# Kernel tuning notes

Hardware: AMD Instinct MI355X
Metric: run time of the kernel (lower is better)

The kernel has to match this reference:

```python
import jax, jax.numpy as jnp
import numpy as np

C = 256
C8 = C // 8  # query/key channels
B, T, W, H = 4, 8, 32, 32


def setup_inputs() -> dict:
    key = jax.random.key(0)
    ks = jax.random.split(key, 8)
    s = 0.05
    return {
        "x": jax.random.normal(ks[0], (B, C, T, W, H), dtype=jnp.float32),
        "wq": jax.random.normal(ks[1], (C8, C), dtype=jnp.float32) * s,
        "bq": jax.random.normal(ks[2], (C8,), dtype=jnp.float32) * s,
        "wk": jax.random.normal(ks[3], (C8, C), dtype=jnp.float32) * s,
        "bk": jax.random.normal(ks[4], (C8,), dtype=jnp.float32) * s,
        "wv": jax.random.normal(ks[5], (C, C), dtype=jnp.float32) * s,
        "bv": jax.random.normal(ks[6], (C,), dtype=jnp.float32) * s,
        "gamma": jax.random.normal(ks[7], (1,), dtype=jnp.float32),
    }


def reference(x, wq, bq, wk, bk, wv, bv, gamma):
    b, c, t, w, h = x.shape
    n = w * h
    # Faithful to torch: x.view(-1, c, w, h) is a row-major reinterpretation
    xr = jnp.reshape(x, (-1, c, n))  # (m, C, N), m = B*T
    # 1x1 convs == per-pixel linear projections
    q = jnp.einsum("oc,mcn->mno", wq, xr) + bq            # (m, N, C8)
    k = jnp.einsum("oc,mcn->mon", wk, xr) + bk[:, None]   # (m, C8, N)
    v = jnp.einsum("oc,mcn->mon", wv, xr) + bv[:, None]   # (m, C, N)
    energy = jnp.einsum("mic,mcj->mij", q, k)             # (m, N, N), unscaled
    attention = jax.nn.softmax(energy, axis=-1)
    out = jnp.einsum("mcn,mnj->mcj", v, attention)        # V @ A (as in torch code)
    out = jnp.reshape(out, (b, c, t, w, h))
    return gamma * out + x
```

## Files before the change

kernel.cpp:

```cpp
#include <hip/hip_runtime.h>

#define MB    32
#define CCH   256
#define QCH   32
#define NPIX  1024
#define SLICE (CCH * NPIX)
#define L2E   1.44269504088896340736f
#define SHIFT 32.0f

typedef __bf16          bf16x8 __attribute__((ext_vector_type(8)));
typedef __bf16          bf16x4 __attribute__((ext_vector_type(4)));
typedef float           f32x4  __attribute__((ext_vector_type(4)));
typedef unsigned int    u32x4  __attribute__((ext_vector_type(4)));
typedef unsigned short  u16x4  __attribute__((ext_vector_type(4)));

__device__ __forceinline__ unsigned short f2bf(float f) {
    unsigned int u = __builtin_bit_cast(unsigned int, f);
    u += 0x7FFFu + ((u >> 16) & 1u);
    return (unsigned short)(u >> 16);
}
__device__ __forceinline__ u16x4 cvt4(float a, float b, float c, float d) {
    bf16x4 v = { (__bf16)a, (__bf16)b, (__bf16)c, (__bf16)d };
    return __builtin_bit_cast(u16x4, v);
}
__device__ __forceinline__ float bf2f(unsigned short u) {
    unsigned int v = (unsigned int)u << 16;
    return __builtin_bit_cast(float, v);
}
__device__ __forceinline__ bf16x8 ldfrag(const unsigned short* p) {
    u32x4 u = *(const u32x4*)p;
    return __builtin_bit_cast(bf16x8, u);
}

#define WB_OFF  0u
#define QT_OFF  262144u
#define KT_OFF  2359296u
#define V_OFF   4456448u
#define A2F_OFF 21233664u
#define PU_OFF  21364736u
#define WS_NEED 88473600u

__global__ __launch_bounds__(256) void k_prep_w(
    const float* __restrict__ wq, const float* __restrict__ wk,
    const float* __restrict__ wv, unsigned short* __restrict__ Wb)
{
    int i4 = (blockIdx.x * 256 + threadIdx.x) * 4;
    int o = i4 >> 8, c = i4 & 255;
    const float* src = (o < 32) ? wq + (size_t)o * CCH + c
                     : (o < 64) ? wk + (size_t)(o - 32) * CCH + c
                                : wv + (size_t)(o - 64) * CCH + c;
    float4 v = *(const float4*)src;
    *(u16x4*)(Wb + i4) = cvt4(v.x, v.y, v.z, v.w);
}

__global__ __launch_bounds__(256) void k_proj(
    const float* __restrict__ x, const unsigned short* __restrict__ Wb,
    const float* __restrict__ bq, const float* __restrict__ bk,
    const float* __restrict__ bv,
    unsigned short* __restrict__ Qt, unsigned short* __restrict__ Kt,
    unsigned short* __restrict__ V)
{
    __shared__ unsigned short Xs[64 * 268];

    const int t = threadIdx.x, lane = t & 63, w = t >> 6;
    const int lj = lane & 15, q = lane >> 4;
    const int n0 = blockIdx.x * 64;
    const int mi = blockIdx.y;
    const float* xp = x + (size_t)mi * SLICE;

#pragma unroll
    for (int r = 0; r < 8; ++r) {
        int job = t + r * 256;
        int cp = job >> 4;
        int seg = job & 15;
        float4 va = *(const float4*)(xp + (size_t)(2 * cp) * NPIX + n0 + seg * 4);
        float4 vb = *(const float4*)(xp + (size_t)(2 * cp + 1) * NPIX + n0 + seg * 4);
        u16x4 da = cvt4(va.x, va.y, va.z, va.w);
        u16x4 db = cvt4(vb.x, vb.y, vb.z, vb.w);
#pragma unroll
        for (int e = 0; e < 4; ++e) {
            unsigned pk = (unsigned)da[e] | ((unsigned)db[e] << 16);
            *(unsigned*)&Xs[(seg * 4 + e) * 268 + 2 * cp] = pk;
        }
    }
    __syncthreads();

    f32x4 acc[5][4];
#pragma unroll
    for (int i = 0; i < 5; ++i)
#pragma unroll
        for (int b = 0; b < 4; ++b) acc[i][b] = (f32x4){0.f, 0.f, 0.f, 0.f};

    const unsigned short* wbase = Wb + (size_t)(w * 16 + lj) * CCH + q * 8;
    const unsigned short* xbase = &Xs[lj * 268 + q * 8];

#pragma unroll 2
    for (int kc = 0; kc < CCH; kc += 32) {
        bf16x8 a[5];
#pragma unroll
        for (int i = 0; i < 5; ++i)
            a[i] = ldfrag(wbase + (size_t)i * 64 * CCH + kc);
        bf16x8 xb[4];
#pragma unroll
        for (int b = 0; b < 4; ++b)
            xb[b] = ldfrag(xbase + b * 16 * 268 + kc);
#pragma unroll
        for (int i = 0; i < 5; ++i)
#pragma unroll
            for (int b = 0; b < 4; ++b)
                acc[i][b] = (i == 0)
                    ? __builtin_amdgcn_mfma_f32_16x16x32_bf16(a[i], xb[b], acc[i][b], 0, 0, 0)
                    : __builtin_amdgcn_mfma_f32_16x16x32_bf16(xb[b], a[i], acc[i][b], 0, 0, 0);
    }

#pragma unroll
    for (int i = 0; i < 5; ++i) {
        if (i == 0) {
            const int ob = w * 16 + 4 * q;
            if (w < 2) {
                unsigned short* Qp = Qt + (size_t)mi * NPIX * QCH;
                float b0 = bq[ob], b1 = bq[ob + 1], b2 = bq[ob + 2], b3 = bq[ob + 3];
#pragma unroll
                for (int b = 0; b < 4; ++b) {
                    int n = n0 + b * 16 + lj;
                    *(u16x4*)(Qp + (size_t)n * QCH + ob) =
                        cvt4((acc[i][b][0] + b0) * L2E, (acc[i][b][1] + b1) * L2E,
                             (acc[i][b][2] + b2) * L2E, (acc[i][b][3] + b3) * L2E);
                }
            } else {
                unsigned short* Kp = Kt + (size_t)mi * NPIX * QCH;
                int o2 = ob - 32;
                float b0 = bk[o2], b1 = bk[o2 + 1], b2 = bk[o2 + 2], b3 = bk[o2 + 3];
#pragma unroll
                for (int b = 0; b < 4; ++b) {
                    int n = n0 + b * 16 + lj;
                    *(u16x4*)(Kp + (size_t)n * QCH + o2) =
                        cvt4(acc[i][b][0] + b0, acc[i][b][1] + b1,
                             acc[i][b][2] + b2, acc[i][b][3] + b3);
                }
            }
        } else {
            unsigned short* Vw = V + (size_t)mi * SLICE;
            const int c16 = w + 4 * (i - 1);
            const float bb = bv[c16 * 16 + lj];
            const int n05 = n0 >> 5;
#pragma unroll
            for (int b = 0; b < 4; ++b) {
                const int l = lj | (((b & 1) * 2 + (q >> 1)) << 4);
                size_t base = ((size_t)(c16 * 32 + n05 + (b >> 1)) * 64 + l) * 8 + (q & 1) * 4;
                *(u16x4*)(Vw + base) = cvt4(acc[i][b][0] + bb, acc[i][b][1] + bb,
                                            acc[i][b][2] + bb, acc[i][b][3] + bb);
            }
        }
    }
}

__global__ __launch_bounds__(256) void k_stats(
    const unsigned short* __restrict__ Qt, const unsigned short* __restrict__ Kt,
    float* __restrict__ a2f)
{
    const int t = threadIdx.x, lane = t & 63, w = t >> 6;
    const int lj = lane & 15, q = lane >> 4;
    const int n16 = blockIdx.x * 64 + w * 16;
    const int mi = blockIdx.y;
    const unsigned short* Qp = Qt + (size_t)mi * NPIX * QCH;
    const unsigned short* Kp = Kt + (size_t)mi * NPIX * QCH;

    bf16x8 qa = ldfrag(Qp + (size_t)(n16 + lj) * QCH + q * 8);

    float s[4] = { 0.f, 0.f, 0.f, 0.f };
#pragma unroll 8
    for (int jc = 0; jc < NPIX; jc += 16) {
        bf16x8 kb = ldfrag(Kp + (size_t)(jc + lj) * QCH + q * 8);
        f32x4 z = (f32x4){0.f, 0.f, 0.f, 0.f};
        f32x4 e = __builtin_amdgcn_mfma_f32_16x16x32_bf16(qa, kb, z, 0, 0, 0);
#pragma unroll
        for (int r = 0; r < 4; ++r) s[r] += exp2f(e[r] - SHIFT);
    }
#pragma unroll
    for (int msk = 1; msk <= 8; msk <<= 1)
#pragma unroll
        for (int r = 0; r < 4; ++r) s[r] += __shfl_xor(s[r], msk, 64);
    if (lj == 0) {
        float* apo = a2f + (size_t)mi * NPIX;
#pragma unroll
        for (int r = 0; r < 4; ++r)
            apo[n16 + 4 * q + r] = SHIFT + log2f(s[r]);
    }
}

__global__ __launch_bounds__(256) void k_pu(
    const unsigned short* __restrict__ Qt, const unsigned short* __restrict__ Kt,
    const float* __restrict__ a2f, unsigned short* __restrict__ Pu)
{
    __shared__ unsigned short Ps[4][32][36];

    const int t = threadIdx.x, lane = t & 63, w = t >> 6;
    const int lj = lane & 15, q = lane >> 4;
    const int nb = blockIdx.x >> 2;
    const int jh = blockIdx.x & 3;
    const int nw = nb * 128 + w * 32;
    const int mi = blockIdx.y;
    const unsigned short* Qp = Qt + (size_t)mi * NPIX * QCH;
    const unsigned short* Kp = Kt + (size_t)mi * NPIX * QCH;
    const float* ap = a2f + (size_t)mi * NPIX;
    unsigned short* Pup = Pu + (size_t)mi * NPIX * NPIX;

    bf16x8 qa[2];
    f32x4  a4[2];
#pragma unroll
    for (int h = 0; h < 2; ++h) {
        qa[h] = ldfrag(Qp + (size_t)(nw + h * 16 + lj) * QCH + q * 8);
        a4[h] = *(const f32x4*)(ap + nw + h * 16 + 4 * q);
    }

    const int jbeg = jh * 256;
#pragma unroll 2
    for (int jc = jbeg; jc < jbeg + 256; jc += 32) {
#pragma unroll
        for (int f = 0; f < 2; ++f) {
            bf16x8 kb = ldfrag(Kp + (size_t)(jc + f * 16 + lj) * QCH + q * 8);
#pragma unroll
            for (int h = 0; h < 2; ++h) {
                f32x4 z = (f32x4){0.f, 0.f, 0.f, 0.f};
                f32x4 e = __builtin_amdgcn_mfma_f32_16x16x32_bf16(qa[h], kb, z, 0, 0, 0);
                *(u16x4*)&Ps[w][f * 16 + lj][h * 16 + 4 * q] =
                    cvt4(exp2f(e[0] - a4[h][0]), exp2f(e[1] - a4[h][1]),
                         exp2f(e[2] - a4[h][2]), exp2f(e[3] - a4[h][3]));
            }
        }
#pragma unroll
        for (int f = 0; f < 2; ++f) {
            u32x4 bfrag = *(const u32x4*)&Ps[w][f * 16 + lj][q * 8];
            *(u32x4*)(Pup + ((size_t)((jc >> 4) + f) * 32 + (nw >> 5)) * 512 + lane * 8) = bfrag;
        }
    }
}

__global__ __launch_bounds__(256, 4) void k_gemm_out(
    const float* __restrict__ x, const float* __restrict__ gamma,
    const unsigned short* __restrict__ Vf, const unsigned short* __restrict__ Pu,
    float* __restrict__ out)
{
    __shared__ unsigned short Vs[2][4096];

    const int b = blockIdx.x;
    const int mi  = (b & 7) | ((b >> 8) << 3);
    const int sub = (b >> 3) & 31;
    const int j0  = (sub & 7) * 128;
    const int cb  = sub >> 3;

    const int t = threadIdx.x, lane = t & 63, w = t >> 6;
    const int lj = lane & 15, q = lane >> 4;
    const int jw = j0 + w * 32;

    const unsigned short* Vp  = Vf + (size_t)mi * SLICE;
    const unsigned short* Pup = Pu + (size_t)mi * NPIX * NPIX
                              + ((size_t)(jw >> 4) * 32) * 512 + lane * 8;

    const int fs = t >> 5;
    const int ln0 = (t & 31) * 2;
    const unsigned short* vsrc0 = Vp
        + ((size_t)((cb * 4 + (fs & 3)) * 32) + (fs >> 2)) * 512 + ln0 * 8;

    f32x4 acc[4][2];
#pragma unroll
    for (int ci = 0; ci < 4; ++ci)
#pragma unroll
        for (int f = 0; f < 2; ++f) acc[ci][f] = (f32x4){0.f, 0.f, 0.f, 0.f};

    {
        u32x4 d0 = *(const u32x4*)vsrc0;
        u32x4 d1 = *(const u32x4*)(vsrc0 + 8);
        *(u32x4*)&Vs[0][fs * 512 + ln0 * 8] = d0;
        *(u32x4*)&Vs[0][fs * 512 + ln0 * 8 + 8] = d1;
    }
    bf16x8 pf[2][2], pfN[2][2];
#pragma unroll
    for (int h = 0; h < 2; ++h)
#pragma unroll
        for (int f = 0; f < 2; ++f) {
            pf[h][f]  = ldfrag(Pup + f * 16384 + (size_t)h * 512);
            pfN[h][f] = ldfrag(Pup + f * 16384 + (size_t)(2 + h) * 512);
        }
    __syncthreads();

    int p = 0;
    for (int nc = 0; nc < NPIX; nc += 64, p ^= 1) {
        const int n1 = (nc + 64) & (NPIX - 1);
        const int n2 = (nc + 128) & (NPIX - 1);
        const unsigned short* vs = vsrc0 + (size_t)(n1 >> 6) * 1024;
        u32x4 nv0 = *(const u32x4*)vs;
        u32x4 nv1 = *(const u32x4*)(vs + 8);
        bf16x8 pf2[2][2];
#pragma unroll
        for (int h = 0; h < 2; ++h)
#pragma unroll
            for (int f = 0; f < 2; ++f)
                pf2[h][f] = ldfrag(Pup + f * 16384 + ((size_t)(n2 >> 5) + h) * 512);

        __builtin_amdgcn_s_setprio(1);
#pragma unroll
        for (int h = 0; h < 2; ++h) {
#pragma unroll
            for (int ci = 0; ci < 4; ++ci) {
                bf16x8 vfr = ldfrag(&Vs[p][(h * 4 + ci) * 512 + lane * 8]);
#pragma unroll
                for (int f = 0; f < 2; ++f)
                    acc[ci][f] = __builtin_amdgcn_mfma_f32_16x16x32_bf16(vfr, pf[h][f], acc[ci][f], 0, 0, 0);
            }
        }
        __builtin_amdgcn_s_setprio(0);

        *(u32x4*)&Vs[p ^ 1][fs * 512 + ln0 * 8] = nv0;
        *(u32x4*)&Vs[p ^ 1][fs * 512 + ln0 * 8 + 8] = nv1;
        __syncthreads();
#pragma unroll
        for (int h = 0; h < 2; ++h)
#pragma unroll
            for (int f = 0; f < 2; ++f) { pf[h][f] = pfN[h][f]; pfN[h][f] = pf2[h][f]; }
    }

    const float g = gamma[0];
    const size_t obase = (size_t)mi * SLICE;
#pragma unroll
    for (int ci = 0; ci < 4; ++ci) {
#pragma unroll
        for (int f = 0; f < 2; ++f) {
#pragma unroll
            for (int r = 0; r < 4; ++r) {
                int c = cb * 64 + ci * 16 + 4 * q + r;
                int j = jw + f * 16 + lj;
                size_t off = obase + (size_t)c * NPIX + j;
                out[off] = g * acc[ci][f][r] + x[off];
            }
        }
    }
}

__global__ __launch_bounds__(256) void k_attn_out(
    const float* __restrict__ x, const float* __restrict__ gamma,
    const unsigned short* __restrict__ Qt, const unsigned short* __restrict__ Kt,
    const unsigned short* __restrict__ Vf, const float* __restrict__ a2f,
    float* __restrict__ out)
{
    __shared__ unsigned short Vs[2][8 * 512];
    __shared__ unsigned short Ps[4][32][36];

    const int b = blockIdx.x;
    const int mi  = (b & 7) | ((b >> 7) << 3);
    const int sub = (b >> 3) & 15;
    const int j0  = (sub & 7) * 128;
    const int cb  = sub >> 3;

    const int t = threadIdx.x, lane = t & 63, w = t >> 6;
    const int lj = lane & 15, q = lane >> 4;
    const int jw = j0 + w * 32;

    const unsigned short* Qp = Qt + (size_t)mi * NPIX * QCH;
    const unsigned short* Kp = Kt + (size_t)mi * NPIX * QCH;
    const unsigned short* Vp = Vf + (size_t)mi * SLICE;
    const float* ap = a2f + (size_t)mi * NPIX;

    bf16x8 kb[2];
#pragma unroll
    for (int sj = 0; sj < 2; ++sj)
        kb[sj] = ldfrag(Kp + (size_t)(jw + sj * 16 + lj) * QCH + q * 8);

    const int ctl = t >> 5, ln0 = (t & 31) * 2;
    const unsigned short* vsrc0 = Vp + ((size_t)(cb * 8 + ctl) * 32) * 512 + ln0 * 8;

    f32x4 acc[8][2];
#pragma unroll
    for (int ci = 0; ci < 8; ++ci)
#pragma unroll
        for (int ji = 0; ji < 2; ++ji) acc[ci][ji] = (f32x4){0.f, 0.f, 0.f, 0.f};

    {
        u32x4 d0 = *(const u32x4*)vsrc0;
        u32x4 d1 = *(const u32x4*)(vsrc0 + 8);
        *(u32x4*)&Vs[0][ctl * 512 + ln0 * 8] = d0;
        *(u32x4*)&Vs[0][ctl * 512 + ln0 * 8 + 8] = d1;
    }
    bf16x8 qa_n[2];
    f32x4  a4_n[2];
#pragma unroll
    for (int sn = 0; sn < 2; ++sn) {
        qa_n[sn] = ldfrag(Qp + (size_t)(sn * 16 + lj) * QCH + q * 8);
        a4_n[sn] = *(const f32x4*)(ap + sn * 16 + 4 * q);
    }
    __syncthreads();

    int p = 0;
    for (int nc = 0; nc < NPIX; nc += 32, p ^= 1) {
        const int nn = (nc + 32) & (NPIX - 1);
        const unsigned short* vsrc = vsrc0 + (size_t)(nn >> 5) * 512;
        u32x4 nv0 = *(const u32x4*)vsrc;
        u32x4 nv1 = *(const u32x4*)(vsrc + 8);

        bf16x8 qa0 = qa_n[0], qa1 = qa_n[1];
        f32x4 a40 = a4_n[0], a41 = a4_n[1];
#pragma unroll
        for (int sj = 0; sj < 2; ++sj) {
            f32x4 z = (f32x4){0.f, 0.f, 0.f, 0.f};
            f32x4 e0 = __builtin_amdgcn_mfma_f32_16x16x32_bf16(qa0, kb[sj], z, 0, 0, 0);
            f32x4 e1 = __builtin_amdgcn_mfma_f32_16x16x32_bf16(qa1, kb[sj], z, 0, 0, 0);
            *(u16x4*)&Ps[w][sj * 16 + lj][4 * q] =
                cvt4(exp2f(e0[0] - a40[0]), exp2f(e0[1] - a40[1]),
                     exp2f(e0[2] - a40[2]), exp2f(e0[3] - a40[3]));
            *(u16x4*)&Ps[w][sj * 16 + lj][16 + 4 * q] =
                cvt4(exp2f(e1[0] - a41[0]), exp2f(e1[1] - a41[1]),
                     exp2f(e1[2] - a41[2]), exp2f(e1[3] - a41[3]));
        }
#pragma unroll
        for (int sn = 0; sn < 2; ++sn) {
            qa_n[sn] = ldfrag(Qp + (size_t)(nn + sn * 16 + lj) * QCH + q * 8);
            a4_n[sn] = *(const f32x4*)(ap + nn + sn * 16 + 4 * q);
        }

        bf16x8 pf[2];
#pragma unroll
        for (int ji = 0; ji < 2; ++ji)
            pf[ji] = ldfrag(&Ps[w][ji * 16 + lj][q * 8]);
#pragma unroll
        for (int ci = 0; ci < 8; ++ci) {
            bf16x8 vfr = ldfrag(&Vs[p][ci * 512 + lane * 8]);
#pragma unroll
            for (int ji = 0; ji < 2; ++ji)
                acc[ci][ji] = __builtin_amdgcn_mfma_f32_16x16x32_bf16(vfr, pf[ji], acc[ci][ji], 0, 0, 0);
        }

        *(u32x4*)&Vs[p ^ 1][ctl * 512 + ln0 * 8] = nv0;
        *(u32x4*)&Vs[p ^ 1][ctl * 512 + ln0 * 8 + 8] = nv1;
        __syncthreads();
    }

    const float g = gamma[0];
    const size_t obase = (size_t)mi * SLICE;
#pragma unroll
    for (int ci = 0; ci < 8; ++ci) {
#pragma unroll
        for (int ji = 0; ji < 2; ++ji) {
#pragma unroll
            for (int r = 0; r < 4; ++r) {
                int c = cb * 128 + ci * 16 + 4 * q + r;
                int j = jw + ji * 16 + lj;
                size_t off = obase + (size_t)c * NPIX + j;
                out[off] = g * acc[ci][ji][r] + x[off];
            }
        }
    }
}

extern "C" void kernel_launch(void* const* d_in, const int* in_sizes, int n_in,
                              void* d_out, int out_size, void* d_ws, size_t ws_size,
                              hipStream_t stream)
{
    const float* x     = (const float*)d_in[0];
    const float* wq    = (const float*)d_in[1];
    const float* bq    = (const float*)d_in[2];
    const float* wk    = (const float*)d_in[3];
    const float* bk    = (const float*)d_in[4];
    const float* wv    = (const float*)d_in[5];
    const float* bv    = (const float*)d_in[6];
    const float* gamma = (const float*)d_in[7];
    float* out = (float*)d_out;

    char* wsb = (char*)d_ws;
    unsigned short* Wb = (unsigned short*)(wsb + WB_OFF);
    unsigned short* Qt = (unsigned short*)(wsb + QT_OFF);
    unsigned short* Kt = (unsigned short*)(wsb + KT_OFF);
    unsigned short* V  = (unsigned short*)(wsb + V_OFF);
    float*          a2 = (float*)(wsb + A2F_OFF);
    unsigned short* Pu = (unsigned short*)(wsb + PU_OFF);

    k_prep_w<<<80, 256, 0, stream>>>(wq, wk, wv, Wb);
    k_proj<<<dim3(NPIX / 64, MB), 256, 0, stream>>>(x, Wb, bq, bk, bv, Qt, Kt, V);
    k_stats<<<dim3(NPIX / 64, MB), 256, 0, stream>>>(Qt, Kt, a2);

    if (ws_size >= (size_t)WS_NEED) {
        k_pu<<<dim3(32, MB), 256, 0, stream>>>(Qt, Kt, a2, Pu);
        k_gemm_out<<<1024, 256, 0, stream>>>(x, gamma, V, Pu, out);
    } else {
        k_attn_out<<<512, 256, 0, stream>>>(x, gamma, Qt, Kt, V, a2, out);
    }
}
```

Measured before the change: 163.1 us.

## Drop materialized P path; use fused attention kernel with 64-pixel double-buffered V tiles

Removes the two-kernel path that writes the full normalized attention matrix to workspace in bf16 and reads it back in a separate GEMM. Every call now runs the fused kernel, which recomputes the attention probabilities on the fly from Q, K and the precomputed log-sum statistics. That kernel now processes 64 pixels per pipeline step instead of 32, with a larger double-buffered V tile, prefetched Q fragments and priority hints around the MFMA loop. The aim is to avoid the large global write and reread of P, at the cost of fewer blocks (512 vs 1024) and more exp work per block.

```diff
diff --git a/kernel.cpp b/kernel.cpp
--- a/kernel.cpp
+++ b/kernel.cpp
@@ -37,8 +37,6 @@
 #define KT_OFF  2359296u
 #define V_OFF   4456448u
 #define A2F_OFF 21233664u
-#define PU_OFF  21364736u
-#define WS_NEED 88473600u
 
 __global__ __launch_bounds__(256) void k_prep_w(
     const float* __restrict__ wq, const float* __restrict__ wk,
@@ -189,162 +187,13 @@
     }
 }
 
-__global__ __launch_bounds__(256) void k_pu(
-    const unsigned short* __restrict__ Qt, const unsigned short* __restrict__ Kt,
-    const float* __restrict__ a2f, unsigned short* __restrict__ Pu)
-{
-    __shared__ unsigned short Ps[4][32][36];
-
-    const int t = threadIdx.x, lane = t & 63, w = t >> 6;
-    const int lj = lane & 15, q = lane >> 4;
-    const int nb = blockIdx.x >> 2;
-    const int jh = blockIdx.x & 3;
-    const int nw = nb * 128 + w * 32;
-    const int mi = blockIdx.y;
-    const unsigned short* Qp = Qt + (size_t)mi * NPIX * QCH;
-    const unsigned short* Kp = Kt + (size_t)mi * NPIX * QCH;
-    const float* ap = a2f + (size_t)mi * NPIX;
-    unsigned short* Pup = Pu + (size_t)mi * NPIX * NPIX;
-
-    bf16x8 qa[2];
-    f32x4  a4[2];
-#pragma unroll
-    for (int h = 0; h < 2; ++h) {
-        qa[h] = ldfrag(Qp + (size_t)(nw + h * 16 + lj) * QCH + q * 8);
-        a4[h] = *(const f32x4*)(ap + nw + h * 16 + 4 * q);
-    }
-
-    const int jbeg = jh * 256;
-#pragma unroll 2
-    for (int jc = jbeg; jc < jbeg + 256; jc += 32) {
-#pragma unroll
-        for (int f = 0; f < 2; ++f) {
-            bf16x8 kb = ldfrag(Kp + (size_t)(jc + f * 16 + lj) * QCH + q * 8);
-#pragma unroll
-            for (int h = 0; h < 2; ++h) {
-                f32x4 z = (f32x4){0.f, 0.f, 0.f, 0.f};
-                f32x4 e = __builtin_amdgcn_mfma_f32_16x16x32_bf16(qa[h], kb, z, 0, 0, 0);
-                *(u16x4*)&Ps[w][f * 16 + lj][h * 16 + 4 * q] =
-                    cvt4(exp2f(e[0] - a4[h][0]), exp2f(e[1] - a4[h][1]),
-                         exp2f(e[2] - a4[h][2]), exp2f(e[3] - a4[h][3]));
-            }
-        }
-#pragma unroll
-        for (int f = 0; f < 2; ++f) {
-            u32x4 bfrag = *(const u32x4*)&Ps[w][f * 16 + lj][q * 8];
-            *(u32x4*)(Pup + ((size_t)((jc >> 4) + f) * 32 + (nw >> 5)) * 512 + lane * 8) = bfrag;
-        }
-    }
-}
-
-__global__ __launch_bounds__(256, 4) void k_gemm_out(
-    const float* __restrict__ x, const float* __restrict__ gamma,
-    const unsigned short* __restrict__ Vf, const unsigned short* __restrict__ Pu,
-    float* __restrict__ out)
-{
-    __shared__ unsigned short Vs[2][4096];
-
-    const int b = blockIdx.x;
-    const int mi  = (b & 7) | ((b >> 8) << 3);
-    const int sub = (b >> 3) & 31;
-    const int j0  = (sub & 7) * 128;
-    const int cb  = sub >> 3;
-
-    const int t = threadIdx.x, lane = t & 63, w = t >> 6;
-    const int lj = lane & 15, q = lane >> 4;
-    const int jw = j0 + w * 32;
-
-    const unsigned short* Vp  = Vf + (size_t)mi * SLICE;
-    const unsigned short* Pup = Pu + (size_t)mi * NPIX * NPIX
-                              + ((size_t)(jw >> 4) * 32) * 512 + lane * 8;
-
-    const int fs = t >> 5;
-    const int ln0 = (t & 31) * 2;
-    const unsigned short* vsrc0 = Vp
-        + ((size_t)((cb * 4 + (fs & 3)) * 32) + (fs >> 2)) * 512 + ln0 * 8;
-
-    f32x4 acc[4][2];
-#pragma unroll
-    for (int ci = 0; ci < 4; ++ci)
-#pragma unroll
-        for (int f = 0; f < 2; ++f) acc[ci][f] = (f32x4){0.f, 0.f, 0.f, 0.f};
-
-    {
-        u32x4 d0 = *(const u32x4*)vsrc0;
-        u32x4 d1 = *(const u32x4*)(vsrc0 + 8);
-        *(u32x4*)&Vs[0][fs * 512 + ln0 * 8] = d0;
-        *(u32x4*)&Vs[0][fs * 512 + ln0 * 8 + 8] = d1;
-    }
-    bf16x8 pf[2][2], pfN[2][2];
-#pragma unroll
-    for (int h = 0; h < 2; ++h)
-#pragma unroll
-        for (int f = 0; f < 2; ++f) {
-            pf[h][f]  = ldfrag(Pup + f * 16384 + (size_t)h * 512);
-            pfN[h][f] = ldfrag(Pup + f * 16384 + (size_t)(2 + h) * 512);
-        }
-    __syncthreads();
-
-    int p = 0;
-    for (int nc = 0; nc < NPIX; nc += 64, p ^= 1) {
-        const int n1 = (nc + 64) & (NPIX - 1);
-        const int n2 = (nc + 128) & (NPIX - 1);
-        const unsigned short* vs = vsrc0 + (size_t)(n1 >> 6) * 1024;
-        u32x4 nv0 = *(const u32x4*)vs;
-        u32x4 nv1 = *(const u32x4*)(vs + 8);
-        bf16x8 pf2[2][2];
-#pragma unroll
-        for (int h = 0; h < 2; ++h)
-#pragma unroll
-            for (int f = 0; f < 2; ++f)
-                pf2[h][f] = ldfrag(Pup + f * 16384 + ((size_t)(n2 >> 5) + h) * 512);
-
-        __builtin_amdgcn_s_setprio(1);
-#pragma unroll
-        for (int h = 0; h < 2; ++h) {
-#pragma unroll
-            for (int ci = 0; ci < 4; ++ci) {
-                bf16x8 vfr = ldfrag(&Vs[p][(h * 4 + ci) * 512 + lane * 8]);
-#pragma unroll
-                for (int f = 0; f < 2; ++f)
-                    acc[ci][f] = __builtin_amdgcn_mfma_f32_16x16x32_bf16(vfr, pf[h][f], acc[ci][f], 0, 0, 0);
-            }
-        }
-        __builtin_amdgcn_s_setprio(0);
-
-        *(u32x4*)&Vs[p ^ 1][fs * 512 + ln0 * 8] = nv0;
-        *(u32x4*)&Vs[p ^ 1][fs * 512 + ln0 * 8 + 8] = nv1;
-        __syncthreads();
-#pragma unroll
-        for (int h = 0; h < 2; ++h)
-#pragma unroll
-            for (int f = 0; f < 2; ++f) { pf[h][f] = pfN[h][f]; pfN[h][f] = pf2[h][f]; }
-    }
-
-    const float g = gamma[0];
-    const size_t obase = (size_t)mi * SLICE;
-#pragma unroll
-    for (int ci = 0; ci < 4; ++ci) {
-#pragma unroll
-        for (int f = 0; f < 2; ++f) {
-#pragma unroll
-            for (int r = 0; r < 4; ++r) {
-                int c = cb * 64 + ci * 16 + 4 * q + r;
-                int j = jw + f * 16 + lj;
-                size_t off = obase + (size_t)c * NPIX + j;
-                out[off] = g * acc[ci][f][r] + x[off];
-            }
-        }
-    }
-}
-
-__global__ __launch_bounds__(256) void k_attn_out(
+__global__ __launch_bounds__(256) void k_fused(
     const float* __restrict__ x, const float* __restrict__ gamma,
     const unsigned short* __restrict__ Qt, const unsigned short* __restrict__ Kt,
     const unsigned short* __restrict__ Vf, const float* __restrict__ a2f,
     float* __restrict__ out)
 {
-    __shared__ unsigned short Vs[2][8 * 512];
+    __shared__ unsigned short Vs[2][8192];
     __shared__ unsigned short Ps[4][32][36];
 
     const int b = blockIdx.x;
@@ -367,8 +216,8 @@
     for (int sj = 0; sj < 2; ++sj)
         kb[sj] = ldfrag(Kp + (size_t)(jw + sj * 16 + lj) * QCH + q * 8);
 
-    const int ctl = t >> 5, ln0 = (t & 31) * 2;
-    const unsigned short* vsrc0 = Vp + ((size_t)(cb * 8 + ctl) * 32) * 512 + ln0 * 8;
+    const int fs = t >> 5, ln0 = (t & 31) * 2;
+    const unsigned short* vsrc0 = Vp + ((size_t)(cb * 8 + fs) * 32) * 512 + ln0 * 8;
 
     f32x4 acc[8][2];
 #pragma unroll
@@ -377,62 +226,82 @@
         for (int ji = 0; ji < 2; ++ji) acc[ci][ji] = (f32x4){0.f, 0.f, 0.f, 0.f};
 
     {
-        u32x4 d0 = *(const u32x4*)vsrc0;
-        u32x4 d1 = *(const u32x4*)(vsrc0 + 8);
-        *(u32x4*)&Vs[0][ctl * 512 + ln0 * 8] = d0;
-        *(u32x4*)&Vs[0][ctl * 512 + ln0 * 8 + 8] = d1;
-    }
-    bf16x8 qa_n[2];
-    f32x4  a4_n[2];
-#pragma unroll
-    for (int sn = 0; sn < 2; ++sn) {
-        qa_n[sn] = ldfrag(Qp + (size_t)(sn * 16 + lj) * QCH + q * 8);
-        a4_n[sn] = *(const f32x4*)(ap + sn * 16 + 4 * q);
-    }
+        u32x4 a0 = *(const u32x4*)(vsrc0);
+        u32x4 a1 = *(const u32x4*)(vsrc0 + 8);
+        u32x4 b0 = *(const u32x4*)(vsrc0 + 512);
+        u32x4 b1 = *(const u32x4*)(vsrc0 + 520);
+        *(u32x4*)&Vs[0][fs * 512 + ln0 * 8]            = a0;
+        *(u32x4*)&Vs[0][fs * 512 + ln0 * 8 + 8]        = a1;
+        *(u32x4*)&Vs[0][4096 + fs * 512 + ln0 * 8]     = b0;
+        *(u32x4*)&Vs[0][4096 + fs * 512 + ln0 * 8 + 8] = b1;
+    }
+    bf16x8 qa[2][2];
+    f32x4  a4[2][2];
+#pragma unroll
+    for (int h = 0; h < 2; ++h)
+#pragma unroll
+        for (int sn = 0; sn < 2; ++sn) {
+            qa[h][sn] = ldfrag(Qp + (size_t)(h * 32 + sn * 16 + lj) * QCH + q * 8);
+            a4[h][sn] = *(const f32x4*)(ap + h * 32 + sn * 16 + 4 * q);
+        }
     __syncthreads();
 
     int p = 0;
-    for (int nc = 0; nc < NPIX; nc += 32, p ^= 1) {
-        const int nn = (nc + 32) & (NPIX - 1);
-        const unsigned short* vsrc = vsrc0 + (size_t)(nn >> 5) * 512;
-        u32x4 nv0 = *(const u32x4*)vsrc;
-        u32x4 nv1 = *(const u32x4*)(vsrc + 8);
-
-        bf16x8 qa0 = qa_n[0], qa1 = qa_n[1];
-        f32x4 a40 = a4_n[0], a41 = a4_n[1];
-#pragma unroll
-        for (int sj = 0; sj < 2; ++sj) {
-            f32x4 z = (f32x4){0.f, 0.f, 0.f, 0.f};
-            f32x4 e0 = __builtin_amdgcn_mfma_f32_16x16x32_bf16(qa0, kb[sj], z, 0, 0, 0);
-            f32x4 e1 = __builtin_amdgcn_mfma_f32_16x16x32_bf16(qa1, kb[sj], z, 0, 0, 0);
-            *(u16x4*)&Ps[w][sj * 16 + lj][4 * q] =
-                cvt4(exp2f(e0[0] - a40[0]), exp2f(e0[1] - a40[1]),
-                     exp2f(e0[2] - a40[2]), exp2f(e0[3] - a40[3]));
-            *(u16x4*)&Ps[w][sj * 16 + lj][16 + 4 * q] =
-                cvt4(exp2f(e1[0] - a41[0]), exp2f(e1[1] - a41[1]),
-                     exp2f(e1[2] - a41[2]), exp2f(e1[3] - a41[3]));
-        }
-#pragma unroll
-        for (int sn = 0; sn < 2; ++sn) {
-            qa_n[sn] = ldfrag(Qp + (size_t)(nn + sn * 16 + lj) * QCH + q * 8);
-            a4_n[sn] = *(const f32x4*)(ap + nn + sn * 16 + 4 * q);
-        }
-
-        bf16x8 pf[2];
-#pragma unroll
-        for (int ji = 0; ji < 2; ++ji)
-            pf[ji] = ldfrag(&Ps[w][ji * 16 + lj][q * 8]);
-#pragma unroll
-        for (int ci = 0; ci < 8; ++ci) {
-            bf16x8 vfr = ldfrag(&Vs[p][ci * 512 + lane * 8]);
+    for (int nc = 0; nc < NPIX; nc += 64, p ^= 1) {
+        const int n1 = (nc + 64) & (NPIX - 1);
+        const unsigned short* vs = vsrc0 + (size_t)(n1 >> 5) * 512;
+        u32x4 nv0 = *(const u32x4*)vs;
+        u32x4 nv1 = *(const u32x4*)(vs + 8);
+        u32x4 nv2 = *(const u32x4*)(vs + 512);
+        u32x4 nv3 = *(const u32x4*)(vs + 520);
+        bf16x8 qa_n[2][2];
+        f32x4  a4_n[2][2];
+#pragma unroll
+        for (int h = 0; h < 2; ++h)
+#pragma unroll
+            for (int sn = 0; sn < 2; ++sn) {
+                qa_n[h][sn] = ldfrag(Qp + (size_t)(n1 + h * 32 + sn * 16 + lj) * QCH + q * 8);
+                a4_n[h][sn] = *(const f32x4*)(ap + n1 + h * 32 + sn * 16 + 4 * q);
+            }
+
+#pragma unroll
+        for (int h = 0; h < 2; ++h) {
+#pragma unroll
+            for (int sj = 0; sj < 2; ++sj) {
+                f32x4 z = (f32x4){0.f, 0.f, 0.f, 0.f};
+                f32x4 e0 = __builtin_amdgcn_mfma_f32_16x16x32_bf16(qa[h][0], kb[sj], z, 0, 0, 0);
+                f32x4 e1 = __builtin_amdgcn_mfma_f32_16x16x32_bf16(qa[h][1], kb[sj], z, 0, 0, 0);
+                *(u16x4*)&Ps[w][sj * 16 + lj][4 * q] =
+                    cvt4(exp2f(e0[0] - a4[h][0][0]), exp2f(e0[1] - a4[h][0][1]),
+                         exp2f(e0[2] - a4[h][0][2]), exp2f(e0[3] - a4[h][0][3]));
+                *(u16x4*)&Ps[w][sj * 16 + lj][16 + 4 * q] =
+                    cvt4(exp2f(e1[0] - a4[h][1][0]), exp2f(e1[1] - a4[h][1][1]),
+                         exp2f(e1[2] - a4[h][1][2]), exp2f(e1[3] - a4[h][1][3]));
+            }
+            bf16x8 pf[2];
 #pragma unroll
             for (int ji = 0; ji < 2; ++ji)
-                acc[ci][ji] = __builtin_amdgcn_mfma_f32_16x16x32_bf16(vfr, pf[ji], acc[ci][ji], 0, 0, 0);
-        }
-
-        *(u32x4*)&Vs[p ^ 1][ctl * 512 + ln0 * 8] = nv0;
-        *(u32x4*)&Vs[p ^ 1][ctl * 512 + ln0 * 8 + 8] = nv1;
+                pf[ji] = ldfrag(&Ps[w][ji * 16 + lj][q * 8]);
+            __builtin_amdgcn_s_setprio(1);
+#pragma unroll
+            for (int ci = 0; ci < 8; ++ci) {
+                bf16x8 vfr = ldfrag(&Vs[p][h * 4096 + ci * 512 + lane * 8]);
+#pragma unroll
+                for (int ji = 0; ji < 2; ++ji)
+                    acc[ci][ji] = __builtin_amdgcn_mfma_f32_16x16x32_bf16(vfr, pf[ji], acc[ci][ji], 0, 0, 0);
+            }
+            __builtin_amdgcn_s_setprio(0);
+        }
+
+        *(u32x4*)&Vs[p ^ 1][fs * 512 + ln0 * 8]            = nv0;
+        *(u32x4*)&Vs[p ^ 1][fs * 512 + ln0 * 8 + 8]        = nv1;
+        *(u32x4*)&Vs[p ^ 1][4096 + fs * 512 + ln0 * 8]     = nv2;
+        *(u32x4*)&Vs[p ^ 1][4096 + fs * 512 + ln0 * 8 + 8] = nv3;
         __syncthreads();
+#pragma unroll
+        for (int h = 0; h < 2; ++h)
+#pragma unroll
+            for (int sn = 0; sn < 2; ++sn) { qa[h][sn] = qa_n[h][sn]; a4[h][sn] = a4_n[h][sn]; }
     }
 
     const float g = gamma[0];
@@ -472,16 +341,9 @@
     unsigned short* Kt = (unsigned short*)(wsb + KT_OFF);
     unsigned short* V  = (unsigned short*)(wsb + V_OFF);
     float*          a2 = (float*)(wsb + A2F_OFF);
-    unsigned short* Pu = (unsigned short*)(wsb + PU_OFF);
 
     k_prep_w<<<80, 256, 0, stream>>>(wq, wk, wv, Wb);
     k_proj<<<dim3(NPIX / 64, MB), 256, 0, stream>>>(x, Wb, bq, bk, bv, Qt, Kt, V);
     k_stats<<<dim3(NPIX / 64, MB), 256, 0, stream>>>(Qt, Kt, a2);
-
-    if (ws_size >= (size_t)WS_NEED) {
-        k_pu<<<dim3(32, MB), 256, 0, stream>>>(Qt, Kt, a2, Pu);
-        k_gemm_out<<<1024, 256, 0, stream>>>(x, gamma, V, Pu, out);
-    } else {
-        k_attn_out<<<512, 256, 0, stream>>>(x, gamma, Qt, Kt, V, a2, out);
-    }
-}
+    k_fused<<<512, 256, 0, stream>>>(x, gamma, Qt, Kt, V, a2, out);
+}
```

New measurement: 169.5 us. 1.04x slower.

## Fuse softmax row-sum into Pu pass and fold normalization into V staging

Applied to the files above, without the earlier changes.

Removes the separate k_stats kernel that recomputed QK^T to find softmax denominators. k_pu now writes unnormalized exp(e-SHIFT) probabilities and accumulates row sums through atomics into a buffer zeroed in k_prep_w. k_gemm_out scales V columns by the reciprocal sums while staging into shared memory. This saves a full QK^T plus exp pass, at the cost of atomics, redundant V scaling per block, and a fixed-shift exponent that could overflow bf16/fp32 range.

```diff
diff --git a/kernel.cpp b/kernel.cpp
--- a/kernel.cpp
+++ b/kernel.cpp
@@ -31,6 +31,17 @@
     u32x4 u = *(const u32x4*)p;
     return __builtin_bit_cast(bf16x8, u);
 }
+__device__ __forceinline__ u32x4 vscale(u32x4 d, const float* __restrict__ r8) {
+    const unsigned short* ds = (const unsigned short*)&d;
+    u16x4 a = cvt4(bf2f(ds[0]) * r8[0], bf2f(ds[1]) * r8[1],
+                   bf2f(ds[2]) * r8[2], bf2f(ds[3]) * r8[3]);
+    u16x4 b = cvt4(bf2f(ds[4]) * r8[4], bf2f(ds[5]) * r8[5],
+                   bf2f(ds[6]) * r8[6], bf2f(ds[7]) * r8[7]);
+    u32x4 o;
+    ((u16x4*)&o)[0] = a;
+    ((u16x4*)&o)[1] = b;
+    return o;
+}
 
 #define WB_OFF  0u
 #define QT_OFF  262144u
@@ -42,15 +53,20 @@
 
 __global__ __launch_bounds__(256) void k_prep_w(
     const float* __restrict__ wq, const float* __restrict__ wk,
-    const float* __restrict__ wv, unsigned short* __restrict__ Wb)
-{
-    int i4 = (blockIdx.x * 256 + threadIdx.x) * 4;
-    int o = i4 >> 8, c = i4 & 255;
-    const float* src = (o < 32) ? wq + (size_t)o * CCH + c
-                     : (o < 64) ? wk + (size_t)(o - 32) * CCH + c
-                                : wv + (size_t)(o - 64) * CCH + c;
-    float4 v = *(const float4*)src;
-    *(u16x4*)(Wb + i4) = cvt4(v.x, v.y, v.z, v.w);
+    const float* __restrict__ wv, unsigned short* __restrict__ Wb,
+    float* __restrict__ S)
+{
+    int tid = blockIdx.x * 256 + threadIdx.x;
+    S[tid] = 0.0f;
+    int i4 = tid * 4;
+    if (i4 < 320 * CCH) {
+        int o = i4 >> 8, c = i4 & 255;
+        const float* src = (o < 32) ? wq + (size_t)o * CCH + c
+                         : (o < 64) ? wk + (size_t)(o - 32) * CCH + c
+                                    : wv + (size_t)(o - 64) * CCH + c;
+        float4 v = *(const float4*)src;
+        *(u16x4*)(Wb + i4) = cvt4(v.x, v.y, v.z, v.w);
+    }
 }
 
 __global__ __launch_bounds__(256) void k_proj(
@@ -191,7 +207,7 @@
 
 __global__ __launch_bounds__(256) void k_pu(
     const unsigned short* __restrict__ Qt, const unsigned short* __restrict__ Kt,
-    const float* __restrict__ a2f, unsigned short* __restrict__ Pu)
+    float* __restrict__ S, unsigned short* __restrict__ Pu)
 {
     __shared__ unsigned short Ps[4][32][36];
 
@@ -203,16 +219,18 @@
     const int mi = blockIdx.y;
     const unsigned short* Qp = Qt + (size_t)mi * NPIX * QCH;
     const unsigned short* Kp = Kt + (size_t)mi * NPIX * QCH;
-    const float* ap = a2f + (size_t)mi * NPIX;
     unsigned short* Pup = Pu + (size_t)mi * NPIX * NPIX;
 
     bf16x8 qa[2];
-    f32x4  a4[2];
-#pragma unroll
-    for (int h = 0; h < 2; ++h) {
+#pragma unroll
+    for (int h = 0; h < 2; ++h)
         qa[h] = ldfrag(Qp + (size_t)(nw + h * 16 + lj) * QCH + q * 8);
-        a4[h] = *(const f32x4*)(ap + nw + h * 16 + 4 * q);
-    }
+
+    float s[2][4];
+#pragma unroll
+    for (int h = 0; h < 2; ++h)
+#pragma unroll
+        for (int r = 0; r < 4; ++r) s[h][r] = 0.f;
 
     const int jbeg = jh * 256;
 #pragma unroll 2
@@ -224,9 +242,10 @@
             for (int h = 0; h < 2; ++h) {
                 f32x4 z = (f32x4){0.f, 0.f, 0.f, 0.f};
                 f32x4 e = __builtin_amdgcn_mfma_f32_16x16x32_bf16(qa[h], kb, z, 0, 0, 0);
-                *(u16x4*)&Ps[w][f * 16 + lj][h * 16 + 4 * q] =
-                    cvt4(exp2f(e[0] - a4[h][0]), exp2f(e[1] - a4[h][1]),
-                         exp2f(e[2] - a4[h][2]), exp2f(e[3] - a4[h][3]));
+                float p0 = exp2f(e[0] - SHIFT), p1 = exp2f(e[1] - SHIFT);
+                float p2 = exp2f(e[2] - SHIFT), p3 = exp2f(e[3] - SHIFT);
+                s[h][0] += p0; s[h][1] += p1; s[h][2] += p2; s[h][3] += p3;
+                *(u16x4*)&Ps[w][f * 16 + lj][h * 16 + 4 * q] = cvt4(p0, p1, p2, p3);
             }
         }
 #pragma unroll
@@ -235,14 +254,30 @@
             *(u32x4*)(Pup + ((size_t)((jc >> 4) + f) * 32 + (nw >> 5)) * 512 + lane * 8) = bfrag;
         }
     }
+
+#pragma unroll
+    for (int msk = 1; msk <= 8; msk <<= 1)
+#pragma unroll
+        for (int h = 0; h < 2; ++h)
+#pragma unroll
+            for (int r = 0; r < 4; ++r) s[h][r] += __shfl_xor(s[h][r], msk, 64);
+    if (lj == 0) {
+        float* Sp = S + (size_t)mi * NPIX;
+#pragma unroll
+        for (int h = 0; h < 2; ++h)
+#pragma unroll
+            for (int r = 0; r < 4; ++r)
+                atomicAdd(&Sp[nw + h * 16 + 4 * q + r], s[h][r]);
+    }
 }
 
 __global__ __launch_bounds__(256, 4) void k_gemm_out(
     const float* __restrict__ x, const float* __restrict__ gamma,
     const unsigned short* __restrict__ Vf, const unsigned short* __restrict__ Pu,
-    float* __restrict__ out)
+    const float* __restrict__ S, float* __restrict__ out)
 {
     __shared__ unsigned short Vs[2][4096];
+    __shared__ float rs[NPIX];
 
     const int b = blockIdx.x;
     const int mi  = (b & 7) | ((b >> 8) << 3);
@@ -254,12 +289,18 @@
     const int lj = lane & 15, q = lane >> 4;
     const int jw = j0 + w * 32;
 
+    const float* Sp = S + (size_t)mi * NPIX;
+#pragma unroll
+    for (int k = 0; k < 4; ++k)
+        rs[t + k * 256] = 1.0f / Sp[t + k * 256];
+
     const unsigned short* Vp  = Vf + (size_t)mi * SLICE;
     const unsigned short* Pup = Pu + (size_t)mi * NPIX * NPIX
                               + ((size_t)(jw >> 4) * 32) * 512 + lane * 8;
 
     const int fs = t >> 5;
     const int ln0 = (t & 31) * 2;
+    const int g8 = (ln0 >> 4) * 8;
     const unsigned short* vsrc0 = Vp
         + ((size_t)((cb * 4 + (fs & 3)) * 32) + (fs >> 2)) * 512 + ln0 * 8;
 
@@ -269,9 +310,12 @@
 #pragma unroll
         for (int f = 0; f < 2; ++f) acc[ci][f] = (f32x4){0.f, 0.f, 0.f, 0.f};
 
+    __syncthreads();
+
     {
-        u32x4 d0 = *(const u32x4*)vsrc0;
-        u32x4 d1 = *(const u32x4*)(vsrc0 + 8);
+        const float* r8 = &rs[(fs >> 2) * 32 + g8];
+        u32x4 d0 = vscale(*(const u32x4*)vsrc0, r8);
+        u32x4 d1 = vscale(*(const u32x4*)(vsrc0 + 8), r8);
         *(u32x4*)&Vs[0][fs * 512 + ln0 * 8] = d0;
         *(u32x4*)&Vs[0][fs * 512 + ln0 * 8 + 8] = d1;
     }
@@ -312,6 +356,11 @@
         }
         __builtin_amdgcn_s_setprio(0);
 
+        {
+            const float* r8 = &rs[((n1 >> 5) + (fs >> 2)) * 32 + g8];
+            nv0 = vscale(nv0, r8);
+            nv1 = vscale(nv1, r8);
+        }
         *(u32x4*)&Vs[p ^ 1][fs * 512 + ln0 * 8] = nv0;
         *(u32x4*)&Vs[p ^ 1][fs * 512 + ln0 * 8 + 8] = nv1;
         __syncthreads();
@@ -471,17 +520,17 @@
     unsigned short* Qt = (unsigned short*)(wsb + QT_OFF);
     unsigned short* Kt = (unsigned short*)(wsb + KT_OFF);
     unsigned short* V  = (unsigned short*)(wsb + V_OFF);
-    float*          a2 = (float*)(wsb + A2F_OFF);
+    float*          Sa = (float*)(wsb + A2F_OFF);
     unsigned short* Pu = (unsigned short*)(wsb + PU_OFF);
 
-    k_prep_w<<<80, 256, 0, stream>>>(wq, wk, wv, Wb);
+    k_prep_w<<<128, 256, 0, stream>>>(wq, wk, wv, Wb, Sa);
     k_proj<<<dim3(NPIX / 64, MB), 256, 0, stream>>>(x, Wb, bq, bk, bv, Qt, Kt, V);
-    k_stats<<<dim3(NPIX / 64, MB), 256, 0, stream>>>(Qt, Kt, a2);
 
     if (ws_size >= (size_t)WS_NEED) {
-        k_pu<<<dim3(32, MB), 256, 0, stream>>>(Qt, Kt, a2, Pu);
-        k_gemm_out<<<1024, 256, 0, stream>>>(x, gamma, V, Pu, out);
+        k_pu<<<dim3(32, MB), 256, 0, stream>>>(Qt, Kt, Sa, Pu);
+        k_gemm_out<<<1024, 256, 0, stream>>>(x, gamma, V, Pu, Sa, out);
     } else {
-        k_attn_out<<<512, 256, 0, stream>>>(x, gamma, Qt, Kt, V, a2, out);
-    }
-}
+        k_stats<<<dim3(NPIX / 64, MB), 256, 0, stream>>>(Qt, Kt, Sa);
+        k_attn_out<<<512, 256, 0, stream>>>(x, gamma, Qt, Kt, V, Sa, out);
+    }
+}
```

Result: faster. 156.0 us (-4.4%).
